# Performance work log

Measured on AMD Instinct MI355X. Metric: run time of the kernel, lower is better.

Reference implementation:

```python
import jax, jax.numpy as jnp
import numpy as np

THRESH = 0.9
NUM_HEADS = 4
HEAD_DIM = 8


def _ln(x, g, b, eps=1e-5):
    m = x.mean(-1, keepdims=True)
    v = ((x - m) ** 2).mean(-1, keepdims=True)
    return (x - m) * jax.lax.rsqrt(v + eps) * g + b


def setup_inputs() -> dict:
    key = jax.random.key(0)
    ks = jax.random.split(key, 32)
    n, d_in, h1, h2, d, ffn, nb = 4096, 512, 128, 64, 32, 64, 2

    def w(k, shape, fan_in):
        return jax.random.normal(k, shape, jnp.float32) * (1.0 / np.sqrt(fan_in))

    inp = {}
    inp["x"] = jax.random.normal(ks[0], (n, d_in), jnp.float32)
    # Autoencoder encoder: input_dim -> 128 -> 64 -> latent_dim
    inp["enc_w1"] = w(ks[1], (d_in, h1), d_in); inp["enc_b1"] = jnp.zeros((h1,), jnp.float32)
    inp["enc_w2"] = w(ks[2], (h1, h2), h1);     inp["enc_b2"] = jnp.zeros((h2,), jnp.float32)
    inp["enc_w3"] = w(ks[3], (h2, d), h2);      inp["enc_b3"] = jnp.zeros((d,), jnp.float32)
    # Transformer blocks (stacked over num_blocks=2)
    inp["wq"] = w(ks[4], (nb, d, d), d); inp["bq"] = jnp.zeros((nb, d), jnp.float32)
    inp["wk"] = w(ks[5], (nb, d, d), d); inp["bk"] = jnp.zeros((nb, d), jnp.float32)
    inp["wv"] = w(ks[6], (nb, d, d), d); inp["bv"] = jnp.zeros((nb, d), jnp.float32)
    inp["wo"] = w(ks[7], (nb, d, d), d); inp["bo"] = jnp.zeros((nb, d), jnp.float32)
    inp["ln1_g"] = jnp.ones((nb, d), jnp.float32);  inp["ln1_b"] = jnp.zeros((nb, d), jnp.float32)
    inp["ffn_w1"] = w(ks[8], (nb, d, ffn), d);      inp["ffn_b1"] = jnp.zeros((nb, ffn), jnp.float32)
    inp["ffn_w2"] = w(ks[9], (nb, ffn, d), ffn);    inp["ffn_b2"] = jnp.zeros((nb, d), jnp.float32)
    inp["ln2_g"] = jnp.ones((nb, d), jnp.float32);  inp["ln2_b"] = jnp.zeros((nb, d), jnp.float32)
    # Head: Linear(d,16) -> Tanh -> Linear(16, num_classes)
    inp["head_w1"] = w(ks[10], (d, 16), d);  inp["head_b1"] = jnp.zeros((16,), jnp.float32)
    inp["head_w2"] = w(ks[11], (16, 1), 16); inp["head_b2"] = jnp.zeros((1,), jnp.float32)
    return inp


def reference(x, enc_w1, enc_b1, enc_w2, enc_b2, enc_w3, enc_b3,
              wq, bq, wk, bk, wv, bv, wo, bo,
              ln1_g, ln1_b, ffn_w1, ffn_b1, ffn_w2, ffn_b2, ln2_g, ln2_b,
              head_w1, head_b1, head_w2, head_b2):
    # --- autoencoder encode: [n, d_in] -> [n, d] ---
    a = jax.nn.relu(x @ enc_w1 + enc_b1)
    a = jax.nn.relu(a @ enc_w2 + enc_b2)
    latent = a @ enc_w3 + enc_b3  # [n, d]

    # --- graph pool: cosine-sim threshold mask, per-node masked neighbor mean ---
    # self-similarity is 1.0 >= THRESH, so every node has >=1 neighbor (deg>=1)
    norms = jnp.linalg.norm(latent, axis=1, keepdims=True) + 1e-12
    normed = latent / norms
    sims = normed @ normed.T                                  # [n, n]
    mask = (sims >= THRESH).astype(latent.dtype)              # [n, n]
    deg = mask.sum(axis=1, keepdims=True)                     # [n, 1]
    pooled = latent + (mask @ latent) / deg                   # latent[i] + mean of neighbors

    # --- transformer blocks (post-LN, eval mode: dropout off) ---
    h = pooled[None]  # [1, n, d]
    n, d = pooled.shape
    nb = wq.shape[0]
    scale = 1.0 / np.sqrt(HEAD_DIM)
    for i in range(nb):
        q = (h @ wq[i] + bq[i]).reshape(1, n, NUM_HEADS, HEAD_DIM)
        k = (h @ wk[i] + bk[i]).reshape(1, n, NUM_HEADS, HEAD_DIM)
        v = (h @ wv[i] + bv[i]).reshape(1, n, NUM_HEADS, HEAD_DIM)
        scores = jnp.einsum('bqhd,bkhd->bhqk', q, k) * scale  # [1, H, n, n]
        attn = jax.nn.softmax(scores, axis=-1)
        o = jnp.einsum('bhqk,bkhd->bqhd', attn, v).reshape(1, n, d)
        o = o @ wo[i] + bo[i]
        h = _ln(h + o, ln1_g[i], ln1_b[i])
        f = jax.nn.relu(h @ ffn_w1[i] + ffn_b1[i]) @ ffn_w2[i] + ffn_b2[i]
        h = _ln(h + f, ln2_g[i], ln2_b[i])

    # --- head on mean-pooled sequence ---
    m = h.mean(axis=1)  # [1, d]
    out = jnp.tanh(m @ head_w1 + head_b1) @ head_w2 + head_b2  # [1, 1]
    return out.squeeze()
```

## Files before the change

kernel.cpp:

```cpp
#include <hip/hip_runtime.h>
#include <math.h>

#define N 4096
#define DIN 512
#define D 32
#define JC 8

typedef float v2f __attribute__((ext_vector_type(2)));
__device__ __forceinline__ v2f fma2(v2f a, float b, v2f c) {
  v2f bb; bb.x = b; bb.y = b;
  return __builtin_elementwise_fma(a, bb, c);
}

__global__ __launch_bounds__(256) void enc_kernel(
    const float* __restrict__ x,
    const float* __restrict__ w1, const float* __restrict__ b1,
    const float* __restrict__ w2, const float* __restrict__ b2,
    const float* __restrict__ w3, const float* __restrict__ b3,
    float* __restrict__ latent, float* __restrict__ normed) {
  __shared__ float xs[8][512];
  __shared__ float h1p[4][8][128];
  __shared__ float h1s[8][128];
  __shared__ float h2s[8][64];
  __shared__ float w2s[128][64];
  __shared__ float w3s[64][32];
  const int t = threadIdx.x;
  const int r0 = blockIdx.x * 8;

  const float4* xg = (const float4*)(x + (size_t)r0 * DIN);
  float4* xl = (float4*)&xs[0][0];
#pragma unroll
  for (int i = 0; i < 4; ++i) xl[t + i * 256] = xg[t + i * 256];
  float4* w2l = (float4*)&w2s[0][0];
  const float4* w2g = (const float4*)w2;
#pragma unroll
  for (int i = 0; i < 8; ++i) w2l[t + i * 256] = w2g[t + i * 256];
  float4* w3l = (float4*)&w3s[0][0];
  const float4* w3g = (const float4*)w3;
#pragma unroll
  for (int i = 0; i < 2; ++i) w3l[t + i * 256] = w3g[t + i * 256];
  __syncthreads();

  {
    const int jc2 = (t & 63) * 2;
    const int kq = t >> 6;
    const int kb = kq * 128;
    float a0[8], a1[8];
#pragma unroll
    for (int r = 0; r < 8; ++r) { a0[r] = 0.f; a1[r] = 0.f; }
    const float* wp = w1 + (size_t)kb * 128 + jc2;

#define ENC_LD4(P0, P1, P2, P3, KK)                          \
    P0 = *(const float2*)&wp[(size_t)(KK) * 128];            \
    P1 = *(const float2*)&wp[(size_t)((KK) + 1) * 128];      \
    P2 = *(const float2*)&wp[(size_t)((KK) + 2) * 128];      \
    P3 = *(const float2*)&wp[(size_t)((KK) + 3) * 128];

#define ENC_STEP(W0, WA, WB, WC, KK)                                   \
    {                                                                  \
      _Pragma("unroll")                                                \
      for (int r = 0; r < 8; ++r) {                                    \
        const float4 xv = *(const float4*)&xs[r][kb + (KK)];           \
        a0[r] = fmaf(xv.x, W0.x, a0[r]); a1[r] = fmaf(xv.x, W0.y, a1[r]); \
        a0[r] = fmaf(xv.y, WA.x, a0[r]); a1[r] = fmaf(xv.y, WA.y, a1[r]); \
        a0[r] = fmaf(xv.z, WB.x, a0[r]); a1[r] = fmaf(xv.z, WB.y, a1[r]); \
        a0[r] = fmaf(xv.w, WC.x, a0[r]); a1[r] = fmaf(xv.w, WC.y, a1[r]); \
      }                                                                \
    }

    float2 A0, A1, A2, A3, B0, B1, B2, B3, C0, C1, C2, C3, D0, D1, D2, D3;
    ENC_LD4(A0, A1, A2, A3, 0)
    ENC_LD4(B0, B1, B2, B3, 4)
    ENC_LD4(C0, C1, C2, C3, 8)
    ENC_LD4(D0, D1, D2, D3, 12)
    for (int kk = 0; kk < 128; kk += 16) {
      ENC_STEP(A0, A1, A2, A3, kk + 0);
      if (kk + 16 < 128) { ENC_LD4(A0, A1, A2, A3, kk + 16) }
      ENC_STEP(B0, B1, B2, B3, kk + 4);
      if (kk + 20 < 128) { ENC_LD4(B0, B1, B2, B3, kk + 20) }
      ENC_STEP(C0, C1, C2, C3, kk + 8);
      if (kk + 24 < 128) { ENC_LD4(C0, C1, C2, C3, kk + 24) }
      ENC_STEP(D0, D1, D2, D3, kk + 12);
      if (kk + 28 < 128) { ENC_LD4(D0, D1, D2, D3, kk + 28) }
    }
#undef ENC_STEP
#undef ENC_LD4
#pragma unroll
    for (int r = 0; r < 8; ++r) {
      h1p[kq][r][jc2] = a0[r];
      h1p[kq][r][jc2 + 1] = a1[r];
    }
  }
  __syncthreads();

#pragma unroll
  for (int e0 = 0; e0 < 1024; e0 += 256) {
    const int e = e0 + t;
    const int r = e >> 7, c = e & 127;
    const float s = b1[c] + ((h1p[0][r][c] + h1p[1][r][c]) + (h1p[2][r][c] + h1p[3][r][c]));
    h1s[r][c] = fmaxf(s, 0.f);
  }
  __syncthreads();

  {
    const int j = t & 63, rg = t >> 6;
    const int ra = rg * 2, rb = ra + 1;
    float a0 = b2[j], a1 = b2[j];
#pragma unroll 8
    for (int kk = 0; kk < 128; ++kk) {
      const float w = w2s[kk][j];
      a0 = fmaf(h1s[ra][kk], w, a0);
      a1 = fmaf(h1s[rb][kk], w, a1);
    }
    h2s[ra][j] = fmaxf(a0, 0.f);
    h2s[rb][j] = fmaxf(a1, 0.f);
  }
  __syncthreads();

  {
    const int j = t & 31, og = t >> 5;
    float acc = b3[j];
#pragma unroll 8
    for (int kk = 0; kk < 64; ++kk) acc = fmaf(h2s[og][kk], w3s[kk][j], acc);
    float s2 = acc * acc;
    s2 += __shfl_xor(s2, 1);
    s2 += __shfl_xor(s2, 2);
    s2 += __shfl_xor(s2, 4);
    s2 += __shfl_xor(s2, 8);
    s2 += __shfl_xor(s2, 16);
    const float inv = 1.0f / (sqrtf(s2) + 1e-12f);
    const size_t off = (size_t)(r0 + og) * D + j;
    latent[off] = acc;
    normed[off] = acc * inv;
  }
}

__global__ __launch_bounds__(256) void pool_kernel(const float* __restrict__ normed,
                                                   const float* __restrict__ latent,
                                                   float* __restrict__ pacc,
                                                   float* __restrict__ pdeg) {
  __shared__ float smem[8192 + 256];
  float* nt = smem;
  float* lt = smem + 4096;
  float* degr = smem + 8192;
  const int t = threadIdx.x;
  const int il = t & 63, g = t >> 6;
  const int i0 = blockIdx.x * 64;
  const int j0 = blockIdx.y * 512;

  float ni[32];
  const float* nrow = normed + (size_t)(i0 + il) * D;
#pragma unroll
  for (int c = 0; c < 32; ++c) ni[c] = nrow[c];

  float acc[32];
#pragma unroll
  for (int c = 0; c < 32; ++c) acc[c] = 0.f;
  float deg = 0.f;

  for (int jt = j0; jt < j0 + 512; jt += 128) {
    __syncthreads();
    const float4* ng = (const float4*)(normed + (size_t)jt * D);
    const float4* lg = (const float4*)(latent + (size_t)jt * D);
    float4* ntl = (float4*)nt;
    float4* ltl = (float4*)lt;
#pragma unroll
    for (int i = 0; i < 4; ++i) {
      ntl[t + i * 256] = ng[t + i * 256];
      ltl[t + i * 256] = lg[t + i * 256];
    }
    __syncthreads();
    for (int jj = g; jj < 128; jj += 4) {
      const float* nr = nt + jj * 32;
      float s = 0.f;
#pragma unroll
      for (int c = 0; c < 32; ++c) s = fmaf(ni[c], nr[c], s);
      if (s >= 0.9f) {
        deg += 1.f;
        const float* lrow = lt + jj * 32;
#pragma unroll
        for (int c = 0; c < 32; ++c) acc[c] += lrow[c];
      }
    }
  }
  __syncthreads();
  float* accr = smem;
#pragma unroll
  for (int c = 0; c < 32; ++c) accr[(g * 64 + il) * 32 + c] = acc[c];
  degr[t] = deg;
  __syncthreads();
  for (int e = t; e < 64 * 32; e += 256) {
    const float s = accr[e] + accr[2048 + e] + accr[4096 + e] + accr[6144 + e];
    pacc[((size_t)blockIdx.y * N + i0 + (e >> 5)) * 32 + (e & 31)] = s;
  }
  if (t < 64) {
    pdeg[(size_t)blockIdx.y * N + i0 + t] = degr[t] + degr[64 + t] + degr[128 + t] + degr[192 + t];
  }
}

__global__ __launch_bounds__(256) void pool_combine(const float* __restrict__ latent,
                                                    const float* __restrict__ pacc,
                                                    const float* __restrict__ pdeg,
                                                    float* __restrict__ h) {
  const int e = blockIdx.x * 256 + threadIdx.x;
  const int i = e >> 5;
  float s = 0.f, dg = 0.f;
#pragma unroll
  for (int gch = 0; gch < JC; ++gch) {
    s += pacc[(size_t)gch * N * 32 + e];
    dg += pdeg[(size_t)gch * N + i];
  }
  h[e] = latent[e] + s / dg;
}

__global__ __launch_bounds__(256) void qkv_kernel(
    const float* __restrict__ h,
    const float* __restrict__ wq, const float* __restrict__ bq,
    const float* __restrict__ wk, const float* __restrict__ bk,
    const float* __restrict__ wv, const float* __restrict__ bv,
    float* __restrict__ q, float* __restrict__ k, float* __restrict__ v,
    int* __restrict__ kmax2i) {
  __shared__ float hs[32][32];
  __shared__ float wsm[3][32][32];
  __shared__ int kred[4];
  const int t = threadIdx.x;
  const int r0 = blockIdx.x * 32;
  if (t < 4) kred[t] = 0;
  ((float4*)&hs[0][0])[t] = ((const float4*)(h + (size_t)r0 * 32))[t];
  ((float4*)&wsm[0][0][0])[t] = ((const float4*)wq)[t];
  ((float4*)&wsm[1][0][0])[t] = ((const float4*)wk)[t];
  ((float4*)&wsm[2][0][0])[t] = ((const float4*)wv)[t];
  __syncthreads();
  const int j = t & 31, og = t >> 5;
  const int head = j >> 3;
  float aq[4], ak[4], av[4];
#pragma unroll
  for (int u = 0; u < 4; ++u) { aq[u] = bq[j]; ak[u] = bk[j]; av[u] = bv[j]; }
  for (int kk = 0; kk < 32; ++kk) {
    const float wqv = wsm[0][kk][j], wkv = wsm[1][kk][j], wvv = wsm[2][kk][j];
#pragma unroll
    for (int u = 0; u < 4; ++u) {
      const float hh = hs[og * 4 + u][kk];
      aq[u] = fmaf(hh, wqv, aq[u]);
      ak[u] = fmaf(hh, wkv, ak[u]);
      av[u] = fmaf(hh, wvv, av[u]);
    }
  }
  const float scale = 1.4426950408889634f * 0.35355339059327373f;
#pragma unroll
  for (int u = 0; u < 4; ++u) {
    const size_t off = (size_t)(r0 + og * 4 + u) * 32 + j;
    q[off] = aq[u] * scale;
    k[off] = ak[u];
    v[off] = av[u];
  }
#pragma unroll
  for (int u = 0; u < 4; ++u) {
    float s2 = ak[u] * ak[u];
    s2 += __shfl_xor(s2, 1);
    s2 += __shfl_xor(s2, 2);
    s2 += __shfl_xor(s2, 4);
    if ((j & 7) == 0) atomicMax(&kred[head], __float_as_int(s2));
  }
  __syncthreads();
  if (t < 4) atomicMax(&kmax2i[t], kred[t]);
}

__global__ __launch_bounds__(256, 4)
void attn_kernel(const float* __restrict__ q,
                 const float* __restrict__ k,
                 const float* __restrict__ v,
                 const int* __restrict__ kmax2i,
                 float* __restrict__ apacc,
                 float* __restrict__ apl) {
  __shared__ float4 tiles[1024];
  float4* kls = tiles;
  float4* vls = tiles + 512;
  const int t = threadIdx.x;
  const int jg = t & 7, head = (t >> 3) & 3, rg = t >> 5;
  const int r0 = blockIdx.x * 32;
  const int j0 = blockIdx.y * (N / JC);

  const float km2 = __int_as_float(kmax2i[head]);

  v2f qq[2][8], acc[2][8], mneg2[2], l2[2];
#pragma unroll
  for (int pr = 0; pr < 2; ++pr) {
    const float* qr0 = q + (size_t)(r0 + rg * 4 + 2 * pr) * 32 + head * 8;
    const float* qr1 = qr0 + 32;
    const float4 qa0 = ((const float4*)qr0)[0], qb0 = ((const float4*)qr0)[1];
    const float4 qa1 = ((const float4*)qr1)[0], qb1 = ((const float4*)qr1)[1];
    qq[pr][0].x = qa0.x; qq[pr][0].y = qa1.x;
    qq[pr][1].x = qa0.y; qq[pr][1].y = qa1.y;
    qq[pr][2].x = qa0.z; qq[pr][2].y = qa1.z;
    qq[pr][3].x = qa0.w; qq[pr][3].y = qa1.w;
    qq[pr][4].x = qb0.x; qq[pr][4].y = qb1.x;
    qq[pr][5].x = qb0.y; qq[pr][5].y = qb1.y;
    qq[pr][6].x = qb0.z; qq[pr][6].y = qb1.z;
    qq[pr][7].x = qb0.w; qq[pr][7].y = qb1.w;
    const float qn0 = qa0.x * qa0.x + qa0.y * qa0.y + qa0.z * qa0.z + qa0.w * qa0.w +
                      qb0.x * qb0.x + qb0.y * qb0.y + qb0.z * qb0.z + qb0.w * qb0.w;
    const float qn1 = qa1.x * qa1.x + qa1.y * qa1.y + qa1.z * qa1.z + qa1.w * qa1.w +
                      qb1.x * qb1.x + qb1.y * qb1.y + qb1.z * qb1.z + qb1.w * qb1.w;
    mneg2[pr].x = -sqrtf(qn0 * km2);
    mneg2[pr].y = -sqrtf(qn1 * km2);
    l2[pr].x = 0.f; l2[pr].y = 0.f;
#pragma unroll
    for (int c = 0; c < 8; ++c) { acc[pr][c].x = 0.f; acc[pr][c].y = 0.f; }
  }

  float4 kr0, kr1, vr0, vr1;
  {
    const float4* kg = (const float4*)(k + (size_t)j0 * 32);
    const float4* vg = (const float4*)(v + (size_t)j0 * 32);
    kr0 = kg[t]; kr1 = kg[t + 256];
    vr0 = vg[t]; vr1 = vg[t + 256];
  }

  const int rA = t >> 3, slotA = (t & 7) ^ (rA & 7);
  const int g1 = t + 256;
  const int rB = g1 >> 3, slotB = (g1 & 7) ^ (rB & 7);

  const int h2 = head * 2;
  const int s0 = h2 ^ jg, s1 = (h2 + 1) ^ jg;
  for (int jt = j0; jt < j0 + (N / JC); jt += 64) {
    __syncthreads();
    kls[rA * 8 + slotA] = kr0;
    kls[rB * 8 + slotB] = kr1;
    vls[rA * 8 + slotA] = vr0;
    vls[rB * 8 + slotB] = vr1;
    __syncthreads();
    if (jt + 64 < j0 + (N / JC)) {
      const float4* kg = (const float4*)(k + (size_t)(jt + 64) * 32);
      const float4* vg = (const float4*)(v + (size_t)(jt + 64) * 32);
      kr0 = kg[t]; kr1 = kg[t + 256];
      vr0 = vg[t]; vr1 = vg[t + 256];
    }
#pragma unroll 2
    for (int it = 0; it < 8; ++it) {
      const int jj = it * 8 + jg;
      const float4 ka = kls[jj * 8 + s0];
      const float4 kb = kls[jj * 8 + s1];
      const float4 va = vls[jj * 8 + s0];
      const float4 vb = vls[jj * 8 + s1];
#pragma unroll
      for (int pr = 0; pr < 2; ++pr) {
        v2f s2 = mneg2[pr];
        s2 = fma2(qq[pr][0], ka.x, s2);
        s2 = fma2(qq[pr][1], ka.y, s2);
        s2 = fma2(qq[pr][2], ka.z, s2);
        s2 = fma2(qq[pr][3], ka.w, s2);
        s2 = fma2(qq[pr][4], kb.x, s2);
        s2 = fma2(qq[pr][5], kb.y, s2);
        s2 = fma2(qq[pr][6], kb.z, s2);
        s2 = fma2(qq[pr][7], kb.w, s2);
        v2f p2;
        p2.x = __builtin_amdgcn_exp2f(s2.x);
        p2.y = __builtin_amdgcn_exp2f(s2.y);
        l2[pr] += p2;
        acc[pr][0] = fma2(p2, va.x, acc[pr][0]);
        acc[pr][1] = fma2(p2, va.y, acc[pr][1]);
        acc[pr][2] = fma2(p2, va.z, acc[pr][2]);
        acc[pr][3] = fma2(p2, va.w, acc[pr][3]);
        acc[pr][4] = fma2(p2, vb.x, acc[pr][4]);
        acc[pr][5] = fma2(p2, vb.y, acc[pr][5]);
        acc[pr][6] = fma2(p2, vb.z, acc[pr][6]);
        acc[pr][7] = fma2(p2, vb.w, acc[pr][7]);
      }
    }
  }
#pragma unroll
  for (int pr = 0; pr < 2; ++pr) {
#pragma unroll
    for (int m = 1; m <= 4; m <<= 1) {
#pragma unroll
      for (int c = 0; c < 8; ++c) {
        acc[pr][c].x += __shfl_xor(acc[pr][c].x, m);
        acc[pr][c].y += __shfl_xor(acc[pr][c].y, m);
      }
      l2[pr].x += __shfl_xor(l2[pr].x, m);
      l2[pr].y += __shfl_xor(l2[pr].y, m);
    }
  }
  if (jg == 0) {
    const size_t abase = (size_t)blockIdx.y * N * 32;
    const size_t lbase = (size_t)blockIdx.y * N * 4;
#pragma unroll
    for (int pr = 0; pr < 2; ++pr) {
      const int row0 = r0 + rg * 4 + 2 * pr;
      float* ap0 = apacc + abase + (size_t)row0 * 32 + head * 8;
      float* ap1 = ap0 + 32;
#pragma unroll
      for (int c = 0; c < 8; ++c) {
        ap0[c] = acc[pr][c].x;
        ap1[c] = acc[pr][c].y;
      }
      apl[lbase + (size_t)row0 * 4 + head] = l2[pr].x;
      apl[lbase + (size_t)(row0 + 1) * 4 + head] = l2[pr].y;
    }
  }
}

__global__ __launch_bounds__(256) void acombine(const float* __restrict__ apacc,
                                                const float* __restrict__ apl,
                                                float* __restrict__ attno) {
  const int e = blockIdx.x * 256 + threadIdx.x;
  const int row = e >> 5;
  const int hh = (e >> 3) & 3;
  float L = 0.f, S = 0.f;
#pragma unroll
  for (int jc = 0; jc < JC; ++jc) {
    L += apl[(size_t)jc * N * 4 + row * 4 + hh];
    S += apacc[(size_t)jc * N * 32 + e];
  }
  attno[e] = S / L;
}

__global__ __launch_bounds__(256) void oln1_kernel(const float* __restrict__ attno,
                                                   const float* __restrict__ wo,
                                                   const float* __restrict__ bo,
                                                   const float* __restrict__ g,
                                                   const float* __restrict__ b,
                                                   float* __restrict__ h) {
  __shared__ float als[32][32];
  __shared__ float wols[32][32];
  __shared__ float ys[32][33];
  const int t = threadIdx.x;
  const int r0 = blockIdx.x * 32;
  ((float4*)&als[0][0])[t] = ((const float4*)(attno + (size_t)r0 * 32))[t];
  ((float4*)&wols[0][0])[t] = ((const float4*)wo)[t];
  __syncthreads();
  const int j = t & 31, og = t >> 5;
  float acc[4];
#pragma unroll
  for (int u = 0; u < 4; ++u) acc[u] = bo[j];
  for (int kk = 0; kk < 32; ++kk) {
    const float w = wols[kk][j];
#pragma unroll
    for (int u = 0; u < 4; ++u) acc[u] = fmaf(als[og * 4 + u][kk], w, acc[u]);
  }
#pragma unroll
  for (int u = 0; u < 4; ++u) {
    const int r = og * 4 + u;
    ys[r][j] = h[(size_t)(r0 + r) * 32 + j] + acc[u];
  }
  __syncthreads();
  if (t < 32) {
    float mu = 0.f;
#pragma unroll
    for (int c = 0; c < 32; ++c) mu += ys[t][c];
    mu *= (1.f / 32.f);
    float var = 0.f;
#pragma unroll
    for (int c = 0; c < 32; ++c) {
      const float dd = ys[t][c] - mu;
      var = fmaf(dd, dd, var);
    }
    var *= (1.f / 32.f);
    const float rs = rsqrtf(var + 1e-5f);
#pragma unroll
    for (int c = 0; c < 32; ++c)
      h[(size_t)(r0 + t) * 32 + c] = (ys[t][c] - mu) * rs * g[c] + b[c];
  }
}

__global__ __launch_bounds__(256) void ffn_kernel(const float* __restrict__ hin,
                                                  const float* __restrict__ w1,
                                                  const float* __restrict__ b1,
                                                  const float* __restrict__ w2,
                                                  const float* __restrict__ b2,
                                                  const float* __restrict__ g,
                                                  const float* __restrict__ bb,
                                                  float* __restrict__ h) {
  __shared__ float hs[32][32];
  __shared__ float w1s[32][64];
  __shared__ float w2s[64][32];
  __shared__ float mids[32][64];
  __shared__ float ys[32][33];
  const int t = threadIdx.x;
  const int r0 = blockIdx.x * 32;
  ((float4*)&hs[0][0])[t] = ((const float4*)(hin + (size_t)r0 * 32))[t];
#pragma unroll
  for (int i = 0; i < 2; ++i) {
    ((float4*)&w1s[0][0])[t + i * 256] = ((const float4*)w1)[t + i * 256];
    ((float4*)&w2s[0][0])[t + i * 256] = ((const float4*)w2)[t + i * 256];
  }
  __syncthreads();
  {
    const int jm = t & 63, gg = t >> 6;
    float acc[8];
#pragma unroll
    for (int u = 0; u < 8; ++u) acc[u] = b1[jm];
    for (int kk = 0; kk < 32; ++kk) {
      const float w = w1s[kk][jm];
#pragma unroll
      for (int u = 0; u < 8; ++u) acc[u] = fmaf(hs[gg * 8 + u][kk], w, acc[u]);
    }
#pragma unroll
    for (int u = 0; u < 8; ++u) mids[gg * 8 + u][jm] = fmaxf(acc[u], 0.f);
  }
  __syncthreads();
  {
    const int j = t & 31, og = t >> 5;
    float acc[4];
#pragma unroll
    for (int u = 0; u < 4; ++u) acc[u] = b2[j];
    for (int kk = 0; kk < 64; ++kk) {
      const float w = w2s[kk][j];
#pragma unroll
      for (int u = 0; u < 4; ++u) acc[u] = fmaf(mids[og * 4 + u][kk], w, acc[u]);
    }
#pragma unroll
    for (int u = 0; u < 4; ++u) {
      const int r = og * 4 + u;
      ys[r][j] = hs[r][j] + acc[u];
    }
  }
  __syncthreads();
  if (t < 32) {
    float mu = 0.f;
#pragma unroll
    for (int c = 0; c < 32; ++c) mu += ys[t][c];
    mu *= (1.f / 32.f);
    float var = 0.f;
#pragma unroll
    for (int c = 0; c < 32; ++c) {
      const float dd = ys[t][c] - mu;
      var = fmaf(dd, dd, var);
    }
    var *= (1.f / 32.f);
    const float rs = rsqrtf(var + 1e-5f);
#pragma unroll
    for (int c = 0; c < 32; ++c)
      h[(size_t)(r0 + t) * 32 + c] = (ys[t][c] - mu) * rs * g[c] + bb[c];
  }
}

__global__ __launch_bounds__(256) void headp_kernel(const float* __restrict__ h,
                                                    float* __restrict__ partial) {
  __shared__ float red[8][32];
  const int t = threadIdx.x;
  const int c = t & 31, rg = t >> 5;
  const int r0 = blockIdx.x * 64;
  float s = 0.f;
#pragma unroll
  for (int u = 0; u < 8; ++u) s += h[(size_t)(r0 + rg * 8 + u) * 32 + c];
  red[rg][c] = s;
  __syncthreads();
  if (t < 32) {
    float ss = 0.f;
#pragma unroll
    for (int u = 0; u < 8; ++u) ss += red[u][t];
    partial[blockIdx.x * 32 + t] = ss;
  }
}

__global__ __launch_bounds__(64) void headf_kernel(const float* __restrict__ partial,
                                                   const float* __restrict__ w1,
                                                   const float* __restrict__ b1,
                                                   const float* __restrict__ w2,
                                                   const float* __restrict__ b2,
                                                   float* __restrict__ out) {
  __shared__ float mls[32];
  __shared__ float tls[16];
  const int t = threadIdx.x;
  if (t < 32) {
    float s = 0.f;
    for (int bb = 0; bb < 64; ++bb) s += partial[bb * 32 + t];
    mls[t] = s * (1.f / 4096.f);
  }
  __syncthreads();
  if (t < 16) {
    float a = b1[t];
#pragma unroll
    for (int c = 0; c < 32; ++c) a = fmaf(mls[c], w1[c * 16 + t], a);
    tls[t] = tanhf(a);
  }
  __syncthreads();
  if (t == 0) {
    float o = b2[0];
#pragma unroll
    for (int jj = 0; jj < 16; ++jj) o = fmaf(tls[jj], w2[jj], o);
    out[0] = o;
  }
}

extern "C" void kernel_launch(void* const* d_in, const int* in_sizes, int n_in,
                              void* d_out, int out_size, void* d_ws, size_t ws_size,
                              hipStream_t stream) {
  const float* x      = (const float*)d_in[0];
  const float* enc_w1 = (const float*)d_in[1];
  const float* enc_b1 = (const float*)d_in[2];
  const float* enc_w2 = (const float*)d_in[3];
  const float* enc_b2 = (const float*)d_in[4];
  const float* enc_w3 = (const float*)d_in[5];
  const float* enc_b3 = (const float*)d_in[6];
  const float* wq     = (const float*)d_in[7];
  const float* bq     = (const float*)d_in[8];
  const float* wk     = (const float*)d_in[9];
  const float* bk     = (const float*)d_in[10];
  const float* wv     = (const float*)d_in[11];
  const float* bv     = (const float*)d_in[12];
  const float* wo     = (const float*)d_in[13];
  const float* bo     = (const float*)d_in[14];
  const float* ln1_g  = (const float*)d_in[15];
  const float* ln1_b  = (const float*)d_in[16];
  const float* ffn_w1 = (const float*)d_in[17];
  const float* ffn_b1 = (const float*)d_in[18];
  const float* ffn_w2 = (const float*)d_in[19];
  const float* ffn_b2 = (const float*)d_in[20];
  const float* ln2_g  = (const float*)d_in[21];
  const float* ln2_b  = (const float*)d_in[22];
  const float* head_w1 = (const float*)d_in[23];
  const float* head_b1 = (const float*)d_in[24];
  const float* head_w2 = (const float*)d_in[25];
  const float* head_b2 = (const float*)d_in[26];

  float* ws      = (float*)d_ws;
  float* latent  = ws;
  float* normed  = ws + 131072;
  float* h       = ws + 262144;
  float* q       = ws + 393216;
  float* k       = ws + 524288;
  float* v       = ws + 655360;
  float* attno   = ws + 786432;
  float* shreg   = ws + 917504;
  float* p_acc   = shreg;
  float* p_deg   = shreg + 1048576;
  float* a_acc   = shreg;
  float* a_l     = shreg + 1048576;
  int*   kmax2i  = (int*)(ws + 2097152);
  float* partial = ws + 2097216;

  hipMemsetAsync(kmax2i, 0, 8 * sizeof(int), stream);

  enc_kernel<<<512, 256, 0, stream>>>(x, enc_w1, enc_b1, enc_w2, enc_b2, enc_w3, enc_b3,
                                      latent, normed);
  pool_kernel<<<dim3(64, JC), 256, 0, stream>>>(normed, latent, p_acc, p_deg);
  pool_combine<<<512, 256, 0, stream>>>(latent, p_acc, p_deg, h);

  for (int blk = 0; blk < 2; ++blk) {
    qkv_kernel<<<128, 256, 0, stream>>>(h, wq + blk * 1024, bq + blk * 32,
                                        wk + blk * 1024, bk + blk * 32,
                                        wv + blk * 1024, bv + blk * 32, q, k, v,
                                        kmax2i + blk * 4);
    attn_kernel<<<dim3(128, JC), 256, 0, stream>>>(q, k, v, kmax2i + blk * 4, a_acc, a_l);
    acombine<<<512, 256, 0, stream>>>(a_acc, a_l, attno);
    oln1_kernel<<<128, 256, 0, stream>>>(attno, wo + blk * 1024, bo + blk * 32,
                                         ln1_g + blk * 32, ln1_b + blk * 32, h);
    ffn_kernel<<<128, 256, 0, stream>>>(h, ffn_w1 + blk * 2048, ffn_b1 + blk * 64,
                                        ffn_w2 + blk * 2048, ffn_b2 + blk * 32,
                                        ln2_g + blk * 32, ln2_b + blk * 32, h);
  }

  headp_kernel<<<64, 256, 0, stream>>>(h, partial);
  headf_kernel<<<1, 64, 0, stream>>>(partial, head_w1, head_b1, head_w2, head_b2, (float*)d_out);
}
```

Baseline: 177.5 us.

## Restructure pool kernel to two rows per thread with packed FMA and shuffle reduction

Each thread in the similarity-pooling kernel now handles two query rows, packed as 2-wide float vectors, so every shared-memory neighbor row it loads feeds two dot products through packed FMA. Eight threads share one row pair, striding over the neighbor tile, and the final reduction uses cross-lane shuffles instead of a shared-memory pass. Occupancy is pinned to two waves per EU to allow the larger register footprint. The extra registers and the branch taken when either row passes the threshold may cost occupancy or add divergence.

```diff
diff --git a/kernel.cpp b/kernel.cpp
--- a/kernel.cpp
+++ b/kernel.cpp
@@ -135,28 +135,31 @@
   }
 }
 
-__global__ __launch_bounds__(256) void pool_kernel(const float* __restrict__ normed,
-                                                   const float* __restrict__ latent,
-                                                   float* __restrict__ pacc,
-                                                   float* __restrict__ pdeg) {
-  __shared__ float smem[8192 + 256];
+__global__ __launch_bounds__(256) __attribute__((amdgpu_waves_per_eu(2, 2)))
+void pool_kernel(const float* __restrict__ normed,
+                 const float* __restrict__ latent,
+                 float* __restrict__ pacc,
+                 float* __restrict__ pdeg) {
+  __shared__ float smem[8192];
   float* nt = smem;
   float* lt = smem + 4096;
-  float* degr = smem + 8192;
-  const int t = threadIdx.x;
-  const int il = t & 63, g = t >> 6;
+  const int t = threadIdx.x;
+  const int jg = t & 7, ip = t >> 3;
   const int i0 = blockIdx.x * 64;
   const int j0 = blockIdx.y * 512;
 
-  float ni[32];
-  const float* nrow = normed + (size_t)(i0 + il) * D;
-#pragma unroll
-  for (int c = 0; c < 32; ++c) ni[c] = nrow[c];
-
-  float acc[32];
-#pragma unroll
-  for (int c = 0; c < 32; ++c) acc[c] = 0.f;
-  float deg = 0.f;
+  v2f nip[32];
+  {
+    const float* nr0 = normed + (size_t)(i0 + ip) * D;
+    const float* nr1 = normed + (size_t)(i0 + ip + 32) * D;
+#pragma unroll
+    for (int c = 0; c < 32; ++c) { nip[c].x = nr0[c]; nip[c].y = nr1[c]; }
+  }
+
+  v2f accp[32], deg2;
+#pragma unroll
+  for (int c = 0; c < 32; ++c) { accp[c].x = 0.f; accp[c].y = 0.f; }
+  deg2.x = 0.f; deg2.y = 0.f;
 
   for (int jt = j0; jt < j0 + 512; jt += 128) {
     __syncthreads();
@@ -170,31 +173,49 @@
       ltl[t + i * 256] = lg[t + i * 256];
     }
     __syncthreads();
-    for (int jj = g; jj < 128; jj += 4) {
-      const float* nr = nt + jj * 32;
-      float s = 0.f;
-#pragma unroll
-      for (int c = 0; c < 32; ++c) s = fmaf(ni[c], nr[c], s);
-      if (s >= 0.9f) {
-        deg += 1.f;
+#pragma unroll 2
+    for (int jj = jg; jj < 128; jj += 8) {
+      const float4* nr = (const float4*)(nt + jj * 32);
+      v2f s2; s2.x = 0.f; s2.y = 0.f;
+#pragma unroll
+      for (int c4 = 0; c4 < 8; ++c4) {
+        const float4 nv = nr[c4];
+        s2 = fma2(nip[c4 * 4 + 0], nv.x, s2);
+        s2 = fma2(nip[c4 * 4 + 1], nv.y, s2);
+        s2 = fma2(nip[c4 * 4 + 2], nv.z, s2);
+        s2 = fma2(nip[c4 * 4 + 3], nv.w, s2);
+      }
+      if (s2.x >= 0.9f || s2.y >= 0.9f) {
+        v2f m2;
+        m2.x = (s2.x >= 0.9f) ? 1.f : 0.f;
+        m2.y = (s2.y >= 0.9f) ? 1.f : 0.f;
+        deg2 += m2;
         const float* lrow = lt + jj * 32;
 #pragma unroll
-        for (int c = 0; c < 32; ++c) acc[c] += lrow[c];
+        for (int c = 0; c < 32; ++c) accp[c] = fma2(m2, lrow[c], accp[c]);
       }
     }
   }
-  __syncthreads();
-  float* accr = smem;
-#pragma unroll
-  for (int c = 0; c < 32; ++c) accr[(g * 64 + il) * 32 + c] = acc[c];
-  degr[t] = deg;
-  __syncthreads();
-  for (int e = t; e < 64 * 32; e += 256) {
-    const float s = accr[e] + accr[2048 + e] + accr[4096 + e] + accr[6144 + e];
-    pacc[((size_t)blockIdx.y * N + i0 + (e >> 5)) * 32 + (e & 31)] = s;
-  }
-  if (t < 64) {
-    pdeg[(size_t)blockIdx.y * N + i0 + t] = degr[t] + degr[64 + t] + degr[128 + t] + degr[192 + t];
+#pragma unroll
+  for (int m = 1; m <= 4; m <<= 1) {
+#pragma unroll
+    for (int c = 0; c < 32; ++c) {
+      accp[c].x += __shfl_xor(accp[c].x, m);
+      accp[c].y += __shfl_xor(accp[c].y, m);
+    }
+    deg2.x += __shfl_xor(deg2.x, m);
+    deg2.y += __shfl_xor(deg2.y, m);
+  }
+  if (jg == 0) {
+    float* pa0 = pacc + ((size_t)blockIdx.y * N + i0 + ip) * 32;
+    float* pa1 = pacc + ((size_t)blockIdx.y * N + i0 + ip + 32) * 32;
+#pragma unroll
+    for (int c = 0; c < 32; ++c) {
+      pa0[c] = accp[c].x;
+      pa1[c] = accp[c].y;
+    }
+    pdeg[(size_t)blockIdx.y * N + i0 + ip] = deg2.x;
+    pdeg[(size_t)blockIdx.y * N + i0 + ip + 32] = deg2.y;
   }
 }
 
```

Measured after the change: 182.3 us. +2.7%, slower.
